# Kernel optimization log

Hardware: AMD Instinct MI355X
Metric: run time of the kernel (lower is better)

## Reference

```python
import jax, jax.numpy as jnp
import numpy as np

N_EMBED = 8192
EMBED_DIM = 256
DECAY = 0.99
EPS = 1e-05


def setup_inputs() -> dict:
    key = jax.random.key(0)
    k1, k2 = jax.random.split(key)
    z = jax.random.normal(k1, (16, 32, 32, EMBED_DIM), dtype=jnp.float32)
    weight = jax.random.normal(k2, (N_EMBED, EMBED_DIM), dtype=jnp.float32)
    cluster_size = jnp.zeros((N_EMBED,), dtype=jnp.float32)
    embed_avg = weight  # register_buffer initialized as a clone of the embedding weight
    return {"z": z, "weight": weight, "cluster_size": cluster_size, "embed_avg": embed_avg}


def reference(z, weight, cluster_size, embed_avg):
    # use_norm=False -> norm is identity; training=True branch; straight_through=True
    zf = z.reshape(-1, EMBED_DIM)  # [N, D]
    # squared euclidean distance: ||z||^2 + ||e||^2 - 2 z.e
    d = (jnp.sum(zf * zf, axis=1, keepdims=True)
         + jnp.sum(weight * weight, axis=1)
         - 2.0 * jnp.einsum('bd,nd->bn', zf, weight))  # [N, K]
    idx = jnp.argmin(d, axis=1)  # [N]
    z_q = weight[idx].reshape(z.shape)
    # commitment loss (z_q detached)
    loss = jnp.mean((jax.lax.stop_gradient(z_q) - z) ** 2)
    # straight-through estimator
    z_q_st = z + jax.lax.stop_gradient(z_q - z)
    # --- EMA codebook update (no_grad in torch) ---
    counts = jax.ops.segment_sum(jnp.ones_like(idx, dtype=jnp.float32), idx, num_segments=N_EMBED)
    dw = jax.ops.segment_sum(zf, idx, num_segments=N_EMBED)  # == onehot.T @ zf
    new_cluster_size = DECAY * cluster_size + (1.0 - DECAY) * counts
    new_embed_avg = DECAY * embed_avg + (1.0 - DECAY) * dw
    n = jnp.sum(new_cluster_size)
    cs = (new_cluster_size + EPS) / (n + N_EMBED * EPS) * n
    new_weight = new_embed_avg / cs[:, None]
    idx_out = idx.reshape(z.shape[:-1])
    return (z_q_st, loss, idx_out,
            jax.lax.stop_gradient(new_weight),
            jax.lax.stop_gradient(new_cluster_size),
            jax.lax.stop_gradient(new_embed_avg))
```

## Files before the change

kernel.cpp:

```cpp
#include <hip/hip_runtime.h>
#include <cstdint>
#include <cstddef>

#define N_PTS   16384
#define K_CODES 8192
#define DIM     256
#define DECAYF  0.99f
#define OMDF    0.01f
#define EPSF    1e-5f

#define OFF_ZQ   0
#define OFF_LOSS 4194304
#define OFF_IDX  4194305
#define OFF_W    4210689
#define OFF_CS   6307841
#define OFF_EA   6316033

#define ZB_OFF   OFF_ZQ
#define WB_OFF   (OFF_ZQ + 2097152)
#define HEN_OFF  (OFF_ZQ + 3145728)
#define C1_OFF   OFF_W
#define C2_OFF   (OFF_W + 1048576)

typedef __attribute__((ext_vector_type(8))) short bf16x8;
typedef __attribute__((ext_vector_type(4))) float f32x4;

__device__ inline unsigned short f2b(float f) {
    unsigned u = __float_as_uint(f);
    return (unsigned short)((u + 0x7FFFu + ((u >> 16) & 1u)) >> 16);
}

__device__ inline unsigned umaxu(unsigned a, unsigned b) { return a > b ? a : b; }
__device__ inline unsigned uminu(unsigned a, unsigned b) { return a < b ? a : b; }

__device__ inline void gload16(const void* g, void* l) {
    __builtin_amdgcn_global_load_lds(
        (const __attribute__((address_space(1))) unsigned int*)g,
        (__attribute__((address_space(3))) unsigned int*)l, 16, 0, 0);
}

__global__ void k_cvt2(const float* __restrict__ z, short* __restrict__ zb,
                       const float* __restrict__ w, short* __restrict__ wb,
                       float* __restrict__ hen, unsigned* __restrict__ cnt) {
    const int tid = threadIdx.x;
    if (blockIdx.x < N_PTS * DIM / 2048) {
        size_t base = (size_t)(blockIdx.x * 256 + tid) * 8;
        float4 a = *(const float4*)(z + base);
        float4 b = *(const float4*)(z + base + 4);
        bf16x8 o;
        o[0] = (short)f2b(128.f * a.x); o[1] = (short)f2b(128.f * a.y);
        o[2] = (short)f2b(128.f * a.z); o[3] = (short)f2b(128.f * a.w);
        o[4] = (short)f2b(128.f * b.x); o[5] = (short)f2b(128.f * b.y);
        o[6] = (short)f2b(128.f * b.z); o[7] = (short)f2b(128.f * b.w);
        *(bf16x8*)(zb + base) = o;
    } else {
        int blk = blockIdx.x - N_PTS * DIM / 2048;
        size_t base = (size_t)(blk * 256 + tid) * 8;
        float4 a = *(const float4*)(w + base);
        float4 b = *(const float4*)(w + base + 4);
        bf16x8 o;
        o[0] = (short)f2b(a.x); o[1] = (short)f2b(a.y);
        o[2] = (short)f2b(a.z); o[3] = (short)f2b(a.w);
        o[4] = (short)f2b(b.x); o[5] = (short)f2b(b.y);
        o[6] = (short)f2b(b.z); o[7] = (short)f2b(b.w);
        *(bf16x8*)(wb + base) = o;
        float s = a.x * a.x + a.y * a.y + a.z * a.z + a.w * a.w
                + b.x * b.x + b.y * b.y + b.z * b.z + b.w * b.w;
        #pragma unroll
        for (int m = 16; m >= 1; m >>= 1) s += __shfl_xor(s, m, 64);
        if ((tid & 31) == 0) hen[base >> 8] = 0.5f * s;
        int gid = blk * 256 + tid;
        if (gid < K_CODES) cnt[gid] = 0u;
    }
}

__global__ __launch_bounds__(256, 4) void k_gemm(const short* __restrict__ zb,
                                                 const short* __restrict__ wb,
                                                 const float* __restrict__ hen,
                                                 unsigned* __restrict__ c1,
                                                 unsigned* __restrict__ c2) {
    __shared__ __align__(16) short As[128 * 64];
    __shared__ __align__(16) short Bs[128 * 64];

    const int tid  = threadIdx.x;
    const int lane = tid & 63;
    const int wv   = tid >> 6;
    const int ztile = blockIdx.x & 127;
    const int kt    = blockIdx.x >> 7;
    const int z0 = ztile * 128, k0 = kt * 128;
    const int col = lane & 15;

    f32x4 acc[2][8];
    #pragma unroll
    for (int ni = 0; ni < 8; ni++) {
        float h = 131072.0f - 128.0f * hen[k0 + ni * 16 + col];
        f32x4 iv = {h, h, h, h};
        acc[0][ni] = iv; acc[1][ni] = iv;
    }
    const unsigned inv0 = (unsigned)(K_CODES - 1 - (k0 + col));

    const int srow = lane >> 3;
    const int scol = ((lane & 7) ^ srow) * 8;

    #pragma unroll
    for (int dc = 0; dc < 4; ++dc) {
        __syncthreads();
        #pragma unroll
        for (int s4 = 0; s4 < 4; ++s4) {
            int seg = wv * 4 + s4;
            gload16(zb + (size_t)(z0 + seg * 8 + srow) * DIM + dc * 64 + scol,
                    As + seg * 512 + lane * 8);
            gload16(wb + (size_t)(k0 + seg * 8 + srow) * DIM + dc * 64 + scol,
                    Bs + seg * 512 + lane * 8);
        }
        __syncthreads();
        #pragma unroll
        for (int kk = 0; kk < 2; ++kk) {
            int ch = ((kk << 2) + (lane >> 4)) ^ (lane & 7);
            bf16x8 a0 = *(const bf16x8*)&As[(wv * 32 + col) * 64 + ch * 8];
            bf16x8 a1 = *(const bf16x8*)&As[(wv * 32 + 16 + col) * 64 + ch * 8];
            #pragma unroll
            for (int ni = 0; ni < 8; ni++) {
                bf16x8 b = *(const bf16x8*)&Bs[(ni * 16 + col) * 64 + ch * 8];
                acc[0][ni] = __builtin_amdgcn_mfma_f32_16x16x32_bf16(
                    a0, b, acc[0][ni], 0, 0, 0);
                acc[1][ni] = __builtin_amdgcn_mfma_f32_16x16x32_bf16(
                    a1, b, acc[1][ni], 0, 0, 0);
            }
        }
    }

    #pragma unroll
    for (int mi = 0; mi < 2; mi++) {
        #pragma unroll
        for (int r = 0; r < 4; r++) {
            unsigned k8[8];
            #pragma unroll
            for (int ni = 0; ni < 8; ni++) {
                unsigned q = (unsigned)acc[mi][ni][r];
                k8[ni] = (q << 13) | (inv0 - 16u * ni);
            }
            unsigned p1 = umaxu(k8[0], k8[1]), q1 = uminu(k8[0], k8[1]);
            unsigned p2 = umaxu(k8[2], k8[3]), q2 = uminu(k8[2], k8[3]);
            unsigned p3 = umaxu(k8[4], k8[5]), q3 = uminu(k8[4], k8[5]);
            unsigned p4 = umaxu(k8[6], k8[7]), q4 = uminu(k8[6], k8[7]);
            unsigned a1 = umaxu(p1, p2);
            unsigned a2 = umaxu(uminu(p1, p2), umaxu(q1, q2));
            unsigned b1 = umaxu(p3, p4);
            unsigned b2 = umaxu(uminu(p3, p4), umaxu(q3, q4));
            unsigned t1 = umaxu(a1, b1);
            unsigned t2 = umaxu(uminu(a1, b1), umaxu(a2, b2));
            unsigned m1 = t1;
            #pragma unroll
            for (int m = 8; m >= 1; m >>= 1)
                m1 = umaxu(m1, (unsigned)__shfl_xor((int)m1, m, 64));
            unsigned cc = (t1 == m1) ? t2 : t1;
            #pragma unroll
            for (int m = 8; m >= 1; m >>= 1)
                cc = umaxu(cc, (unsigned)__shfl_xor((int)cc, m, 64));
            if (col == 0) {
                int row = wv * 32 + mi * 16 + (lane >> 4) * 4 + r;
                c1[(size_t)kt * N_PTS + z0 + row] = m1;
                c2[(size_t)kt * N_PTS + z0 + row] = cc;
            }
        }
    }
}

__global__ __launch_bounds__(256) void k_rescore(
        const float* __restrict__ z, const float* __restrict__ w,
        const unsigned* __restrict__ c1, const unsigned* __restrict__ c2,
        float* __restrict__ out,
        unsigned* __restrict__ cnt, float* __restrict__ lossp) {
    int wid  = (blockIdx.x * 256 + threadIdx.x) >> 6;
    int lane = threadIdx.x & 63;
    float4 zv  = *(const float4*)(z + (size_t)wid * DIM + lane * 4);
    unsigned k1 = c1[(size_t)lane * N_PTS + wid];
    unsigned k2 = c2[(size_t)lane * N_PTS + wid];

    unsigned m1 = k1;
    #pragma unroll
    for (int m = 32; m >= 1; m >>= 1)
        m1 = umaxu(m1, (unsigned)__shfl_xor((int)m1, m, 64));
    unsigned e = (k1 == m1) ? k2 : k1;
    unsigned m2 = e;
    #pragma unroll
    for (int m = 32; m >= 1; m >>= 1)
        m2 = umaxu(m2, (unsigned)__shfl_xor((int)m2, m, 64));

    int idx = K_CODES - 1 - (int)(m1 & 0x1FFFu);
    float4 bw = *(const float4*)(w + (size_t)idx * DIM + lane * 4);

    unsigned qthr = (m1 >> 13) - 96u;
    if ((m2 >> 13) >= qthr) {
        unsigned long long best = 0ULL;
        #pragma unroll
        for (int j = 0; j < 2; j++) {
            unsigned cj = j ? k2 : k1;
            unsigned long long mask = __ballot((cj >> 13) >= qthr);
            while (mask) {
                int l = __ffsll((unsigned long long)mask) - 1;
                mask &= mask - 1;
                unsigned cwd = (unsigned)__shfl((int)cj, l, 64);
                int k = K_CODES - 1 - (int)(cwd & 0x1FFFu);
                float4 wv = *(const float4*)(w + (size_t)k * DIM + lane * 4);
                float s = zv.x * wv.x + zv.y * wv.y + zv.z * wv.z + zv.w * wv.w;
                float h = wv.x * wv.x + wv.y * wv.y + wv.z * wv.z + wv.w * wv.w;
                #pragma unroll
                for (int m = 32; m >= 1; m >>= 1) {
                    s += __shfl_xor(s, m, 64);
                    h += __shfl_xor(h, m, 64);
                }
                float sc = s - 0.5f * h;
                unsigned u = __float_as_uint(sc);
                u = (u & 0x80000000u) ? ~u : (u | 0x80000000u);
                unsigned long long key = ((unsigned long long)u << 32)
                                       | (unsigned)(K_CODES - 1 - k);
                if (key > best) best = key;
            }
        }
        int nidx = K_CODES - 1 - (int)(unsigned)(best & 0xFFFFFFFFull);
        if (nidx != idx) {
            idx = nidx;
            bw = *(const float4*)(w + (size_t)idx * DIM + lane * 4);
        }
    }

    *(float4*)(out + OFF_ZQ + (size_t)wid * DIM + lane * 4) = bw;

    float dx = bw.x - zv.x, dy = bw.y - zv.y, dz = bw.z - zv.z, dw = bw.w - zv.w;
    float s2 = dx * dx + dy * dy + dz * dz + dw * dw;
    #pragma unroll
    for (int m = 32; m >= 1; m >>= 1) s2 += __shfl_xor(s2, m, 64);

    if (lane == 0) {
        out[OFF_IDX + wid] = (float)idx;
        lossp[wid] = s2;
        atomicAdd(cnt + idx, 1u);
    }
}

__global__ __launch_bounds__(1024) void k_prefix(const float* __restrict__ csin,
                                                 float* __restrict__ out,
                                                 const unsigned* __restrict__ cnt,
                                                 unsigned* __restrict__ offs,
                                                 unsigned* __restrict__ list,
                                                 const float* __restrict__ lossp,
                                                 float* __restrict__ nval) {
    __shared__ unsigned scur[K_CODES];
    __shared__ unsigned wtot[16], wbase[16];
    __shared__ float fred[16], fred2[16];
    int t = threadIdx.x, lane = t & 63, wv = t >> 6;
    int base = t * 8;
    unsigned c[8], mysum = 0;
    #pragma unroll
    for (int i = 0; i < 8; i++) { c[i] = cnt[base + i]; mysum += c[i]; }
    unsigned inc = mysum;
    #pragma unroll
    for (int off = 1; off < 64; off <<= 1) {
        unsigned v = (unsigned)__shfl_up((int)inc, off, 64);
        if (lane >= off) inc += v;
    }
    if (lane == 63) wtot[wv] = inc;
    __syncthreads();
    if (t == 0) {
        unsigned r = 0;
        for (int i = 0; i < 16; i++) { wbase[i] = r; r += wtot[i]; }
        offs[K_CODES] = r;
    }
    __syncthreads();
    unsigned my0 = wbase[wv] + inc - mysum;
    float csl = 0.f;
    #pragma unroll
    for (int i = 0; i < 8; i++) {
        offs[base + i] = my0;
        scur[base + i] = my0;
        my0 += c[i];
        float ncs = DECAYF * csin[base + i] + OMDF * (float)c[i];
        out[OFF_CS + base + i] = ncs;
        csl += ncs;
    }
    #pragma unroll
    for (int m = 32; m >= 1; m >>= 1) csl += __shfl_xor(csl, m, 64);
    if (lane == 0) fred[wv] = csl;
    float lp = 0.f;
    #pragma unroll
    for (int i = 0; i < 16; i++) lp += lossp[t + i * 1024];
    #pragma unroll
    for (int m = 32; m >= 1; m >>= 1) lp += __shfl_xor(lp, m, 64);
    if (lane == 0) fred2[wv] = lp;
    __syncthreads();
    if (t == 0) {
        float n = 0.f, L = 0.f;
        for (int i = 0; i < 16; i++) { n += fred[i]; L += fred2[i]; }
        *nval = n;
        out[OFF_LOSS] = L * (1.0f / ((float)N_PTS * DIM));
    }
    for (int i = t; i < N_PTS; i += 1024) {
        int idx = (int)out[OFF_IDX + i];
        unsigned pos = atomicAdd(&scur[idx], 1u);
        list[pos] = (unsigned)i;
    }
}

__global__ void k_gather(const float* __restrict__ z, const float* __restrict__ ea,
                         float* __restrict__ out,
                         const unsigned* __restrict__ offs,
                         const unsigned* __restrict__ list,
                         const float* __restrict__ nval) {
    int k = blockIdx.x, lane = threadIdx.x;
    unsigned beg = offs[k], end = offs[k + 1];
    float4 acc = {0.f, 0.f, 0.f, 0.f};
    for (unsigned p = beg; p < end; ++p) {
        unsigned i = list[p];
        float4 zv = *(const float4*)(z + (size_t)i * DIM + lane * 4);
        acc.x += zv.x; acc.y += zv.y; acc.z += zv.z; acc.w += zv.w;
    }
    float4 e = *(const float4*)(ea + (size_t)k * DIM + lane * 4);
    e.x = DECAYF * e.x + OMDF * acc.x;
    e.y = DECAYF * e.y + OMDF * acc.y;
    e.z = DECAYF * e.z + OMDF * acc.z;
    e.w = DECAYF * e.w + OMDF * acc.w;
    *(float4*)(out + OFF_EA + (size_t)k * DIM + lane * 4) = e;

    float cs = out[OFF_CS + k];
    float n  = *nval;
    float inv = 1.f / ((cs + EPSF) / (n + (float)K_CODES * EPSF) * n);
    float4 wr = {e.x * inv, e.y * inv, e.z * inv, e.w * inv};
    *(float4*)(out + OFF_W + (size_t)k * DIM + lane * 4) = wr;
}

extern "C" void kernel_launch(void* const* d_in, const int* in_sizes, int n_in,
                              void* d_out, int out_size, void* d_ws, size_t ws_size,
                              hipStream_t stream) {
    const float* z  = (const float*)d_in[0];
    const float* w  = (const float*)d_in[1];
    const float* cs = (const float*)d_in[2];
    const float* ea = (const float*)d_in[3];
    float* out = (float*)d_out;

    short*    zb  = (short*)(out + ZB_OFF);
    short*    wb  = (short*)(out + WB_OFF);
    float*    hen = out + HEN_OFF;
    unsigned* c1  = (unsigned*)(out + C1_OFF);
    unsigned* c2  = (unsigned*)(out + C2_OFF);

    unsigned* cnt   = (unsigned*)d_ws;
    unsigned* offs  = cnt + 8192;
    unsigned* list  = offs + 8200;
    float*    lossp = (float*)(list + 16384);
    float*    nval  = lossp + 16384;

    hipLaunchKernelGGL(k_cvt2,    dim3((N_PTS + K_CODES) * DIM / 2048), dim3(256), 0, stream,
                       z, zb, w, wb, hen, cnt);
    hipLaunchKernelGGL(k_gemm,    dim3((N_PTS / 128) * (K_CODES / 128)), dim3(256), 0, stream,
                       zb, wb, hen, c1, c2);
    hipLaunchKernelGGL(k_rescore, dim3(N_PTS / 4),            dim3(256), 0, stream,
                       z, w, c1, c2, out, cnt, lossp);
    hipLaunchKernelGGL(k_prefix,  dim3(1),                    dim3(1024), 0, stream,
                       cs, out, cnt, offs, list, lossp, nval);
    hipLaunchKernelGGL(k_gather,  dim3(K_CODES),              dim3(64), 0, stream,
                       z, ea, out, offs, list, nval);
}
```

Baseline: 289.4 us.

## Enlarge GEMM z-tile to 256 rows and coalesce rescore candidate loads via LDS

The distance GEMM now processes 256 z rows per block (4 MFMA row groups per wave) against 128 codes, so each loaded codebook tile is reused across twice as many rows and the grid is halved. Occupancy hint drops to 2 blocks per CU to make room for the larger accumulator set. The rescore kernel now runs 16 points per 1024-thread block and stages the per-tile top-2 candidates into padded shared memory with coalesced reads, instead of each lane doing strided global reads. The trade-off is higher register and LDS pressure and fewer resident waves for latency hiding in the GEMM.

```diff
diff --git a/kernel.cpp b/kernel.cpp
--- a/kernel.cpp
+++ b/kernel.cpp
@@ -74,28 +74,29 @@
     }
 }
 
-__global__ __launch_bounds__(256, 4) void k_gemm(const short* __restrict__ zb,
+__global__ __launch_bounds__(256, 2) void k_gemm(const short* __restrict__ zb,
                                                  const short* __restrict__ wb,
                                                  const float* __restrict__ hen,
                                                  unsigned* __restrict__ c1,
                                                  unsigned* __restrict__ c2) {
-    __shared__ __align__(16) short As[128 * 64];
+    __shared__ __align__(16) short As[256 * 64];
     __shared__ __align__(16) short Bs[128 * 64];
 
     const int tid  = threadIdx.x;
     const int lane = tid & 63;
     const int wv   = tid >> 6;
-    const int ztile = blockIdx.x & 127;
-    const int kt    = blockIdx.x >> 7;
-    const int z0 = ztile * 128, k0 = kt * 128;
+    const int ztile = blockIdx.x & 63;
+    const int kt    = blockIdx.x >> 6;
+    const int z0 = ztile * 256, k0 = kt * 128;
     const int col = lane & 15;
 
-    f32x4 acc[2][8];
+    f32x4 acc[4][8];
     #pragma unroll
     for (int ni = 0; ni < 8; ni++) {
         float h = 131072.0f - 128.0f * hen[k0 + ni * 16 + col];
         f32x4 iv = {h, h, h, h};
-        acc[0][ni] = iv; acc[1][ni] = iv;
+        #pragma unroll
+        for (int mi = 0; mi < 4; mi++) acc[mi][ni] = iv;
     }
     const unsigned inv0 = (unsigned)(K_CODES - 1 - (k0 + col));
 
@@ -106,10 +107,14 @@
     for (int dc = 0; dc < 4; ++dc) {
         __syncthreads();
         #pragma unroll
+        for (int s8 = 0; s8 < 8; ++s8) {
+            int seg = wv * 8 + s8;
+            gload16(zb + (size_t)(z0 + seg * 8 + srow) * DIM + dc * 64 + scol,
+                    As + seg * 512 + lane * 8);
+        }
+        #pragma unroll
         for (int s4 = 0; s4 < 4; ++s4) {
             int seg = wv * 4 + s4;
-            gload16(zb + (size_t)(z0 + seg * 8 + srow) * DIM + dc * 64 + scol,
-                    As + seg * 512 + lane * 8);
             gload16(wb + (size_t)(k0 + seg * 8 + srow) * DIM + dc * 64 + scol,
                     Bs + seg * 512 + lane * 8);
         }
@@ -117,21 +122,23 @@
         #pragma unroll
         for (int kk = 0; kk < 2; ++kk) {
             int ch = ((kk << 2) + (lane >> 4)) ^ (lane & 7);
-            bf16x8 a0 = *(const bf16x8*)&As[(wv * 32 + col) * 64 + ch * 8];
-            bf16x8 a1 = *(const bf16x8*)&As[(wv * 32 + 16 + col) * 64 + ch * 8];
+            bf16x8 af[4];
+            #pragma unroll
+            for (int mi = 0; mi < 4; mi++)
+                af[mi] = *(const bf16x8*)&As[(wv * 64 + mi * 16 + col) * 64 + ch * 8];
             #pragma unroll
             for (int ni = 0; ni < 8; ni++) {
                 bf16x8 b = *(const bf16x8*)&Bs[(ni * 16 + col) * 64 + ch * 8];
-                acc[0][ni] = __builtin_amdgcn_mfma_f32_16x16x32_bf16(
-                    a0, b, acc[0][ni], 0, 0, 0);
-                acc[1][ni] = __builtin_amdgcn_mfma_f32_16x16x32_bf16(
-                    a1, b, acc[1][ni], 0, 0, 0);
+                #pragma unroll
+                for (int mi = 0; mi < 4; mi++)
+                    acc[mi][ni] = __builtin_amdgcn_mfma_f32_16x16x32_bf16(
+                        af[mi], b, acc[mi][ni], 0, 0, 0);
             }
         }
     }
 
     #pragma unroll
-    for (int mi = 0; mi < 2; mi++) {
+    for (int mi = 0; mi < 4; mi++) {
         #pragma unroll
         for (int r = 0; r < 4; r++) {
             unsigned k8[8];
@@ -159,7 +166,7 @@
             for (int m = 8; m >= 1; m >>= 1)
                 cc = umaxu(cc, (unsigned)__shfl_xor((int)cc, m, 64));
             if (col == 0) {
-                int row = wv * 32 + mi * 16 + (lane >> 4) * 4 + r;
+                int row = wv * 64 + mi * 16 + (lane >> 4) * 4 + r;
                 c1[(size_t)kt * N_PTS + z0 + row] = m1;
                 c2[(size_t)kt * N_PTS + z0 + row] = cc;
             }
@@ -167,16 +174,26 @@
     }
 }
 
-__global__ __launch_bounds__(256) void k_rescore(
+__global__ __launch_bounds__(1024) void k_rescore(
         const float* __restrict__ z, const float* __restrict__ w,
         const unsigned* __restrict__ c1, const unsigned* __restrict__ c2,
         float* __restrict__ out,
         unsigned* __restrict__ cnt, float* __restrict__ lossp) {
-    int wid  = (blockIdx.x * 256 + threadIdx.x) >> 6;
-    int lane = threadIdx.x & 63;
+    __shared__ unsigned s1[64 * 17], s2[64 * 17];
+    const int t  = threadIdx.x;
+    const int w0 = blockIdx.x * 16;
+    {
+        int kt = t >> 4, wo = t & 15;
+        s1[kt * 17 + wo] = c1[(size_t)kt * N_PTS + w0 + wo];
+        s2[kt * 17 + wo] = c2[(size_t)kt * N_PTS + w0 + wo];
+    }
+    __syncthreads();
+    const int wv   = t >> 6;
+    const int lane = t & 63;
+    const int wid  = w0 + wv;
     float4 zv  = *(const float4*)(z + (size_t)wid * DIM + lane * 4);
-    unsigned k1 = c1[(size_t)lane * N_PTS + wid];
-    unsigned k2 = c2[(size_t)lane * N_PTS + wid];
+    unsigned k1 = s1[lane * 17 + wv];
+    unsigned k2 = s2[lane * 17 + wv];
 
     unsigned m1 = k1;
     #pragma unroll
@@ -203,9 +220,9 @@
                 mask &= mask - 1;
                 unsigned cwd = (unsigned)__shfl((int)cj, l, 64);
                 int k = K_CODES - 1 - (int)(cwd & 0x1FFFu);
-                float4 wv = *(const float4*)(w + (size_t)k * DIM + lane * 4);
-                float s = zv.x * wv.x + zv.y * wv.y + zv.z * wv.z + zv.w * wv.w;
-                float h = wv.x * wv.x + wv.y * wv.y + wv.z * wv.z + wv.w * wv.w;
+                float4 wr = *(const float4*)(w + (size_t)k * DIM + lane * 4);
+                float s = zv.x * wr.x + zv.y * wr.y + zv.z * wr.z + zv.w * wr.w;
+                float h = wr.x * wr.x + wr.y * wr.y + wr.z * wr.z + wr.w * wr.w;
                 #pragma unroll
                 for (int m = 32; m >= 1; m >>= 1) {
                     s += __shfl_xor(s, m, 64);
@@ -229,13 +246,13 @@
     *(float4*)(out + OFF_ZQ + (size_t)wid * DIM + lane * 4) = bw;
 
     float dx = bw.x - zv.x, dy = bw.y - zv.y, dz = bw.z - zv.z, dw = bw.w - zv.w;
-    float s2 = dx * dx + dy * dy + dz * dz + dw * dw;
-    #pragma unroll
-    for (int m = 32; m >= 1; m >>= 1) s2 += __shfl_xor(s2, m, 64);
+    float s2v = dx * dx + dy * dy + dz * dz + dw * dw;
+    #pragma unroll
+    for (int m = 32; m >= 1; m >>= 1) s2v += __shfl_xor(s2v, m, 64);
 
     if (lane == 0) {
         out[OFF_IDX + wid] = (float)idx;
-        lossp[wid] = s2;
+        lossp[wid] = s2v;
         atomicAdd(cnt + idx, 1u);
     }
 }
@@ -353,9 +370,9 @@
 
     hipLaunchKernelGGL(k_cvt2,    dim3((N_PTS + K_CODES) * DIM / 2048), dim3(256), 0, stream,
                        z, zb, w, wb, hen, cnt);
-    hipLaunchKernelGGL(k_gemm,    dim3((N_PTS / 128) * (K_CODES / 128)), dim3(256), 0, stream,
+    hipLaunchKernelGGL(k_gemm,    dim3((N_PTS / 256) * (K_CODES / 128)), dim3(256), 0, stream,
                        zb, wb, hen, c1, c2);
-    hipLaunchKernelGGL(k_rescore, dim3(N_PTS / 4),            dim3(256), 0, stream,
+    hipLaunchKernelGGL(k_rescore, dim3(N_PTS / 16),           dim3(1024), 0, stream,
                        z, w, c1, c2, out, cnt, lossp);
     hipLaunchKernelGGL(k_prefix,  dim3(1),                    dim3(1024), 0, stream,
                        cs, out, cnt, offs, list, lossp, nval);
```

After: 294.2 us. About the same (+1.6%).

## Move z_q write into gather, derive loss algebraically, coalesce candidate loads via LDS

Applied to the files above, without the earlier changes.

The rescore kernel no longer loads z and the chosen codeword per point or writes z_q. The loss is computed as ||z||^2 - 2*score, using per-row squared norms precomputed in the conversion kernel. The z_q rows are written in the gather kernel, which already walks each code's point list, so each codeword row is loaded once and scattered. Candidate keys are staged through shared memory with 1024-thread blocks so the c1/c2 reads coalesce. The trade-offs are that the loss now uses the quantized GEMM score when no rescore happens, which is an approximation, and that the gather kernel now issues scattered writes.

```diff
diff --git a/kernel.cpp b/kernel.cpp
--- a/kernel.cpp
+++ b/kernel.cpp
@@ -41,7 +41,8 @@
 
 __global__ void k_cvt2(const float* __restrict__ z, short* __restrict__ zb,
                        const float* __restrict__ w, short* __restrict__ wb,
-                       float* __restrict__ hen, unsigned* __restrict__ cnt) {
+                       float* __restrict__ hen, unsigned* __restrict__ cnt,
+                       float* __restrict__ zn2) {
     const int tid = threadIdx.x;
     if (blockIdx.x < N_PTS * DIM / 2048) {
         size_t base = (size_t)(blockIdx.x * 256 + tid) * 8;
@@ -53,6 +54,11 @@
         o[4] = (short)f2b(128.f * b.x); o[5] = (short)f2b(128.f * b.y);
         o[6] = (short)f2b(128.f * b.z); o[7] = (short)f2b(128.f * b.w);
         *(bf16x8*)(zb + base) = o;
+        float s = a.x * a.x + a.y * a.y + a.z * a.z + a.w * a.w
+                + b.x * b.x + b.y * b.y + b.z * b.z + b.w * b.w;
+        #pragma unroll
+        for (int m = 16; m >= 1; m >>= 1) s += __shfl_xor(s, m, 64);
+        if ((tid & 31) == 0) zn2[blockIdx.x * 8 + (tid >> 5)] = s;
     } else {
         int blk = blockIdx.x - N_PTS * DIM / 2048;
         size_t base = (size_t)(blk * 256 + tid) * 8;
@@ -167,16 +173,26 @@
     }
 }
 
-__global__ __launch_bounds__(256) void k_rescore(
+__global__ __launch_bounds__(1024) void k_rescore(
         const float* __restrict__ z, const float* __restrict__ w,
         const unsigned* __restrict__ c1, const unsigned* __restrict__ c2,
+        const float* __restrict__ zn2,
         float* __restrict__ out,
         unsigned* __restrict__ cnt, float* __restrict__ lossp) {
-    int wid  = (blockIdx.x * 256 + threadIdx.x) >> 6;
-    int lane = threadIdx.x & 63;
-    float4 zv  = *(const float4*)(z + (size_t)wid * DIM + lane * 4);
-    unsigned k1 = c1[(size_t)lane * N_PTS + wid];
-    unsigned k2 = c2[(size_t)lane * N_PTS + wid];
+    __shared__ unsigned s1[64 * 17], s2[64 * 17];
+    const int t  = threadIdx.x;
+    const int w0 = blockIdx.x * 16;
+    {
+        int kt = t >> 4, wo = t & 15;
+        s1[kt * 17 + wo] = c1[(size_t)kt * N_PTS + w0 + wo];
+        s2[kt * 17 + wo] = c2[(size_t)kt * N_PTS + w0 + wo];
+    }
+    __syncthreads();
+    const int wv   = t >> 6;
+    const int lane = t & 63;
+    const int wid  = w0 + wv;
+    unsigned k1 = s1[lane * 17 + wv];
+    unsigned k2 = s2[lane * 17 + wv];
 
     unsigned m1 = k1;
     #pragma unroll
@@ -189,11 +205,12 @@
         m2 = umaxu(m2, (unsigned)__shfl_xor((int)m2, m, 64));
 
     int idx = K_CODES - 1 - (int)(m1 & 0x1FFFu);
-    float4 bw = *(const float4*)(w + (size_t)idx * DIM + lane * 4);
+    float scf = ((float)(int)(m1 >> 13) - 131072.0f) * 0.0078125f;
 
     unsigned qthr = (m1 >> 13) - 96u;
     if ((m2 >> 13) >= qthr) {
         unsigned long long best = 0ULL;
+        float bsc = 0.f;
         #pragma unroll
         for (int j = 0; j < 2; j++) {
             unsigned cj = j ? k2 : k1;
@@ -203,9 +220,14 @@
                 mask &= mask - 1;
                 unsigned cwd = (unsigned)__shfl((int)cj, l, 64);
                 int k = K_CODES - 1 - (int)(cwd & 0x1FFFu);
-                float4 wv = *(const float4*)(w + (size_t)k * DIM + lane * 4);
-                float s = zv.x * wv.x + zv.y * wv.y + zv.z * wv.z + zv.w * wv.w;
-                float h = wv.x * wv.x + wv.y * wv.y + wv.z * wv.z + wv.w * wv.w;
+                float4 wr = *(const float4*)(w + (size_t)k * DIM + lane * 4);
+                float s = 0.f, h = 0.f;
+                {
+                    const float* zr = z + (size_t)wid * DIM + lane * 4;
+                    float4 zv = *(const float4*)zr;
+                    s = zv.x * wr.x + zv.y * wr.y + zv.z * wr.z + zv.w * wr.w;
+                    h = wr.x * wr.x + wr.y * wr.y + wr.z * wr.z + wr.w * wr.w;
+                }
                 #pragma unroll
                 for (int m = 32; m >= 1; m >>= 1) {
                     s += __shfl_xor(s, m, 64);
@@ -216,26 +238,18 @@
                 u = (u & 0x80000000u) ? ~u : (u | 0x80000000u);
                 unsigned long long key = ((unsigned long long)u << 32)
                                        | (unsigned)(K_CODES - 1 - k);
-                if (key > best) best = key;
+                bool better = key > best;
+                best = better ? key : best;
+                bsc  = better ? sc  : bsc;
             }
         }
-        int nidx = K_CODES - 1 - (int)(unsigned)(best & 0xFFFFFFFFull);
-        if (nidx != idx) {
-            idx = nidx;
-            bw = *(const float4*)(w + (size_t)idx * DIM + lane * 4);
-        }
-    }
-
-    *(float4*)(out + OFF_ZQ + (size_t)wid * DIM + lane * 4) = bw;
-
-    float dx = bw.x - zv.x, dy = bw.y - zv.y, dz = bw.z - zv.z, dw = bw.w - zv.w;
-    float s2 = dx * dx + dy * dy + dz * dz + dw * dw;
-    #pragma unroll
-    for (int m = 32; m >= 1; m >>= 1) s2 += __shfl_xor(s2, m, 64);
+        idx = K_CODES - 1 - (int)(unsigned)(best & 0xFFFFFFFFull);
+        scf = bsc;
+    }
 
     if (lane == 0) {
         out[OFF_IDX + wid] = (float)idx;
-        lossp[wid] = s2;
+        lossp[wid] = zn2[wid] - 2.0f * scf;
         atomicAdd(cnt + idx, 1u);
     }
 }
@@ -304,17 +318,20 @@
 }
 
 __global__ void k_gather(const float* __restrict__ z, const float* __restrict__ ea,
+                         const float* __restrict__ w,
                          float* __restrict__ out,
                          const unsigned* __restrict__ offs,
                          const unsigned* __restrict__ list,
                          const float* __restrict__ nval) {
     int k = blockIdx.x, lane = threadIdx.x;
     unsigned beg = offs[k], end = offs[k + 1];
+    float4 wv = *(const float4*)(w + (size_t)k * DIM + lane * 4);
     float4 acc = {0.f, 0.f, 0.f, 0.f};
     for (unsigned p = beg; p < end; ++p) {
         unsigned i = list[p];
         float4 zv = *(const float4*)(z + (size_t)i * DIM + lane * 4);
         acc.x += zv.x; acc.y += zv.y; acc.z += zv.z; acc.w += zv.w;
+        *(float4*)(out + OFF_ZQ + (size_t)i * DIM + lane * 4) = wv;
     }
     float4 e = *(const float4*)(ea + (size_t)k * DIM + lane * 4);
     e.x = DECAYF * e.x + OMDF * acc.x;
@@ -350,15 +367,16 @@
     unsigned* list  = offs + 8200;
     float*    lossp = (float*)(list + 16384);
     float*    nval  = lossp + 16384;
+    float*    zn2   = nval + 1;
 
     hipLaunchKernelGGL(k_cvt2,    dim3((N_PTS + K_CODES) * DIM / 2048), dim3(256), 0, stream,
-                       z, zb, w, wb, hen, cnt);
+                       z, zb, w, wb, hen, cnt, zn2);
     hipLaunchKernelGGL(k_gemm,    dim3((N_PTS / 128) * (K_CODES / 128)), dim3(256), 0, stream,
                        zb, wb, hen, c1, c2);
-    hipLaunchKernelGGL(k_rescore, dim3(N_PTS / 4),            dim3(256), 0, stream,
-                       z, w, c1, c2, out, cnt, lossp);
+    hipLaunchKernelGGL(k_rescore, dim3(N_PTS / 16),           dim3(1024), 0, stream,
+                       z, w, c1, c2, zn2, out, cnt, lossp);
     hipLaunchKernelGGL(k_prefix,  dim3(1),                    dim3(1024), 0, stream,
                        cs, out, cnt, offs, list, lossp, nval);
     hipLaunchKernelGGL(k_gather,  dim3(K_CODES),              dim3(64), 0, stream,
-                       z, ea, out, offs, list, nval);
-}
+                       z, ea, w, out, offs, list, nval);
+}
```

Result: faster. 278.0 us (-4.0%).
